# Performance work log

Hardware: AMD Instinct MI355X
Metric: run time of the kernel (lower is better)

Reference implementation:

```python
import jax, jax.numpy as jnp
import numpy as np

K, B, D, H, C, T = 3, 512, 1024, 512, 48, 25  # num_TAB, batch, linear_dim, hidden, n_classes, max_len

def setup_inputs() -> dict:
    key = jax.random.key(0)
    ks = jax.random.split(key, 18)
    rn = lambda k, s, sc=0.02: (jax.random.normal(k, s, jnp.float32) * sc)
    return {
        'S_ppps': jax.random.normal(ks[0], (K, B, D), jnp.float32),
        'R_ppps': jax.random.normal(ks[1], (K, B, D), jnp.float32),
        'cls_W': rn(ks[2], (K, 2 * D, C)), 'cls_b': jnp.zeros((K, C), jnp.float32),
        'dur_W': rn(ks[3], (K * D, 1)), 'dur_b': jnp.zeros((1,), jnp.float32),
        'lin_W': rn(ks[4], (2 * K * D + K * C, D + 1)), 'lin_b': jnp.zeros((D + 1,), jnp.float32),
        'W_ih': rn(ks[5], (4 * H, D + 1)), 'W_hh': rn(ks[6], (4 * H, H)),
        'b_ih': jnp.zeros((4 * H,), jnp.float32), 'b_hh': jnp.zeros((4 * H,), jnp.float32),
        'Wp': rn(ks[7], (H, C)), 'bp': jnp.zeros((C,), jnp.float32),
        'Wdur': rn(ks[8], (D + H, 1)), 'bdur': jnp.zeros((1,), jnp.float32),
        'embed': rn(ks[9], (C, D), 1.0),
        'Wattn': rn(ks[10], (H, D)),
    }

def reference(S_ppps, R_ppps, cls_W, cls_b, dur_W, dur_b, lin_W, lin_b,
              W_ih, W_hh, b_ih, b_hh, Wp, bp, Wdur, bdur, embed, Wattn):
    S_stack = jnp.transpose(S_ppps, (1, 0, 2))            # [B,K,D] (torch.stack(S_ppps,1))
    # per-TAB classifiers: Y[i] = softmax(Linear(cat(S_i,R_i)))
    SR = jnp.concatenate([S_ppps, R_ppps], axis=-1)       # [K,B,2D]
    Y = jax.nn.softmax(jnp.einsum('kbd,kdc->kbc', SR, cls_W) + cls_b[:, None, :], axis=-1)  # [K,B,C]
    Yf = jnp.transpose(Y, (1, 0, 2)).reshape(B, K * C)    # cat(Y0..Yk) feature-wise
    Sf = jnp.transpose(S_ppps, (1, 0, 2)).reshape(B, K * D)
    Rf = jnp.transpose(R_ppps, (1, 0, 2)).reshape(B, K * D)
    feat = jnp.concatenate([Yf, Sf, Rf], axis=1)          # [B, K*C + 2*K*D]
    x0 = feat @ lin_W + lin_b                             # [B, D+1]
    curr_dur = Rf @ dur_W + dur_b                         # [B,1]
    inv_sqrt_d = 1.0 / np.sqrt(D).astype(np.float32)

    def step(carry, _):
        x, h, c, prev_h = carry
        gates = x @ W_ih.T + b_ih + h @ W_hh.T + b_hh     # [B,4H], torch gate order i,f,g,o
        i_g, f_g, g_g, o_g = jnp.split(gates, 4, axis=1)
        c = jax.nn.sigmoid(f_g) * c + jax.nn.sigmoid(i_g) * jnp.tanh(g_g)
        h = jax.nn.sigmoid(o_g) * jnp.tanh(c)
        logits = h @ Wp + bp                              # [B,C]
        q = (h @ Wattn) * inv_sqrt_d                      # [B,D]
        aw = jax.nn.softmax(jnp.einsum('bd,bkd->bk', q, S_stack), axis=-1)
        att = jnp.einsum('bk,bkd->bd', aw, S_stack)       # [B,D]
        dur = jnp.concatenate([att, prev_h], axis=1) @ Wdur + bdur  # [B,1]
        labels = jnp.argmax(logits, axis=1)
        probs = jax.nn.softmax(logits, axis=1)
        nx = jnp.concatenate([embed[labels], dur], axis=1)  # [B,D+1]
        return (nx, h, c, h), (labels, probs, dur[:, 0], att)

    z = jnp.zeros((B, H), x0.dtype)
    _, (labels_t, probs_t, dur_t, att_t) = jax.lax.scan(step, (x0, z, z, z), None, length=T)
    curr_action = jnp.sum(Y, axis=0)                      # [B,C]
    pred_class_probs = jnp.transpose(probs_t, (1, 0, 2))  # [B,T,C]
    pred_action_durations = jnp.concatenate([curr_dur, dur_t.T], axis=1)  # [B,T+1]
    return (labels_t, pred_class_probs, curr_action, pred_action_durations, att_t)
```

## Files before the change

kernel.cpp:

```cpp
#include <hip/hip_runtime.h>
#include <math.h>

#define B 512
#define D 1024
#define H 512
#define C 48
#define K 3
#define T 25
#define DP1 1025
#define G4H 2048
#define NC 2112
#define NCV 2096
#define KP 1056
#define FK 6304

typedef _Float16 f16;
typedef _Float16 half8 __attribute__((ext_vector_type(8)));
typedef float floatx4 __attribute__((ext_vector_type(4)));

__device__ __forceinline__ float sigf(float x){ return 1.0f/(1.0f+expf(-x)); }


template<int MODE>
__device__ __forceinline__ void mf_load(
    const f16* __restrict__ Ahi, const f16* __restrict__ Alo,
    const f16* __restrict__ Bhi, const f16* __restrict__ Blo,
    int M, int lda, int ldb, int m0, int n0, int kbase, int k0, int t,
    const f16* __restrict__ Yh, const f16* __restrict__ Yl,
    const float* __restrict__ Sf, const float* __restrict__ Rf,
    half8& rah, half8& ral, half8& rbh, half8& rbl)
{
    int r = t>>2, seg = t&3;
    int kk = k0 + seg*8;
    {
        size_t off = (size_t)(n0+r)*ldb + kbase + kk;
        rbh = *(const half8*)(Bhi + off);
        rbl = *(const half8*)(Blo + off);
    }
    int m = m0 + r;
    if (MODE==0){
        if (m < M){
            size_t off = (size_t)m*lda + kbase + kk;
            rah = *(const half8*)(Ahi + off);
            ral = *(const half8*)(Alo + off);
        } else {
            #pragma unroll
            for (int i=0;i<8;i++){ rah[i]=(f16)0; ral[i]=(f16)0; }
        }
    } else {
        int kabs = kbase + kk;
        if (kabs < 144){
            rah = *(const half8*)(Yh + (size_t)m*144 + kabs);
            ral = *(const half8*)(Yl + (size_t)m*144 + kabs);
        } else if (kabs < 6288){
            int kp = kabs - 144;
            const float* src = (kp < 3*D)
                ? (Sf + (size_t)(kp>>10)*(B*D) + (size_t)m*D + (kp&(D-1)))
                : (Rf + (size_t)((kp-3*D)>>10)*(B*D) + (size_t)m*D + ((kp-3*D)&(D-1)));
            float4 f0 = *(const float4*)src;
            float4 f1 = *(const float4*)(src+4);
            float fv[8]={f0.x,f0.y,f0.z,f0.w,f1.x,f1.y,f1.z,f1.w};
            #pragma unroll
            for (int i=0;i<8;i++){
                f16 h=(f16)fv[i];
                rah[i]=h; ral[i]=(f16)(fv[i]-(float)h);
            }
        } else {
            #pragma unroll
            for (int i=0;i<8;i++){ rah[i]=(f16)0; ral[i]=(f16)0; }
        }
    }
}

template<int MODE>
__global__ __launch_bounds__(256)
void k_mfma(const f16* __restrict__ Ahi, const f16* __restrict__ Alo,
            const f16* __restrict__ Bhi, const f16* __restrict__ Blo,
            float* __restrict__ Cc, const float* __restrict__ bias,
            int M, int Nvalid, int Ktot, int lda, int ldb, int ldc,
            int ksl, size_t cstride, int MB, int Z, int zmaj,
            const f16* __restrict__ Yh, const f16* __restrict__ Yl,
            const float* __restrict__ Sf, const float* __restrict__ Rf)
{
    __shared__ __align__(16) f16 Ash[2][64][40];
    __shared__ __align__(16) f16 Asl[2][64][40];
    __shared__ __align__(16) f16 Bsh[2][64][40];
    __shared__ __align__(16) f16 Bsl[2][64][40];
    int t = threadIdx.x;
    int mblk, nblk, z;
    if (zmaj){
        z = blockIdx.x % Z;
        int rest = blockIdx.x / Z;
        mblk = rest % MB; nblk = rest / MB;
    } else {
        int chunk = gridDim.x >> 3;
        int g = (blockIdx.x & 7)*chunk + (blockIdx.x >> 3);
        int mz = g % (MB*Z);
        nblk = g / (MB*Z);
        mblk = mz / Z;
        z    = mz % Z;
    }
    int m0 = mblk*64, n0 = nblk*64;
    int kbase = z*ksl;
    int kcnt = (z==Z-1)? (Ktot-kbase) : ksl;
    int nIter = kcnt >> 5;
    int r = t>>2, seg = t&3;
    half8 rah, ral, rbh, rbl;
    mf_load<MODE>(Ahi,Alo,Bhi,Blo,M,lda,ldb,m0,n0,kbase,0,t,Yh,Yl,Sf,Rf,rah,ral,rbh,rbl);
    int lane = t&63, wv = t>>6;
    int lrow = lane&15, quad = lane>>4;
    floatx4 acc[4] = {};
    int cur = 0;
    for (int it=0; it<nIter; ++it){
        *(half8*)&Ash[cur][r][seg*8] = rah;
        *(half8*)&Asl[cur][r][seg*8] = ral;
        *(half8*)&Bsh[cur][r][seg*8] = rbh;
        *(half8*)&Bsl[cur][r][seg*8] = rbl;
        if (it+1 < nIter)
            mf_load<MODE>(Ahi,Alo,Bhi,Blo,M,lda,ldb,m0,n0,kbase,(it+1)<<5,t,Yh,Yl,Sf,Rf,rah,ral,rbh,rbl);
        __syncthreads();
        half8 ah = *(const half8*)&Ash[cur][wv*16+lrow][quad*8];
        half8 al = *(const half8*)&Asl[cur][wv*16+lrow][quad*8];
        #pragma unroll
        for (int j=0;j<4;j++){
            half8 bh = *(const half8*)&Bsh[cur][j*16+lrow][quad*8];
            half8 bl = *(const half8*)&Bsl[cur][j*16+lrow][quad*8];
            acc[j] = __builtin_amdgcn_mfma_f32_16x16x32_f16(ah, bh, acc[j], 0,0,0);
            acc[j] = __builtin_amdgcn_mfma_f32_16x16x32_f16(al, bh, acc[j], 0,0,0);
            acc[j] = __builtin_amdgcn_mfma_f32_16x16x32_f16(ah, bl, acc[j], 0,0,0);
        }
        cur ^= 1;
    }
    float* Cz = Cc + (size_t)z*cstride;
    #pragma unroll
    for (int j=0;j<4;j++){
        int col = n0 + j*16 + lrow;
        if (col >= Nvalid) continue;
        float bv = bias ? bias[col] : 0.f;
        #pragma unroll
        for (int i=0;i<4;i++){
            int row = m0 + wv*16 + quad*4 + i;
            if (row < M) Cz[(size_t)row*ldc + col] = acc[j][i] + bv;
        }
    }
}


__global__ void k_bt_build(const float* __restrict__ src, f16* __restrict__ hi, f16* __restrict__ lo,
                           int Ksrc, int Nsrc, int ld_src, int NB, int KB, float scale){
    __shared__ float tile[32][33];
    int k0 = blockIdx.x*32, n0 = blockIdx.y*32;
    int lx = threadIdx.x & 31, ly = threadIdx.x >> 5;
    for (int rr=0; rr<32; rr+=8){
        int k2 = k0+ly+rr, n = n0+lx;
        tile[ly+rr][lx] = (k2<Ksrc && n<Nsrc)? src[(size_t)k2*ld_src+n]*scale : 0.f;
    }
    __syncthreads();
    for (int rr=0; rr<32; rr+=8){
        int n = n0+ly+rr, k2 = k0+lx;
        if (n<NB && k2<KB){
            float v = tile[lx][ly+rr];
            f16 h=(f16)v;
            hi[(size_t)n*KB+k2]=h;
            lo[(size_t)n*KB+k2]=(f16)(v-(float)h);
        }
    }
}

__global__ void k_permrows(const float* __restrict__ src, f16* __restrict__ hi, f16* __restrict__ lo,
                           int src_ld, int dst_ld, int kvalid){
    int idx = blockIdx.x*256+threadIdx.x;
    if (idx >= G4H*dst_ld) return;
    int p = idx/dst_ld, k2 = idx%dst_ld;
    int j = p>>2, g = p&3, gi = (g<<9)|j;
    float v = (k2<kvalid)? src[(size_t)gi*src_ld + k2] : 0.f;
    f16 h=(f16)v;
    hi[idx]=h; lo[idx]=(f16)(v-(float)h);
}

__global__ void k_cvt(const float* __restrict__ src, f16* __restrict__ hi, f16* __restrict__ lo,
                      int M, int ld_src, int nvalid, int ld_dst, float scale){
    int idx = blockIdx.x*256+threadIdx.x;
    if (idx >= M*ld_dst) return;
    int m = idx/ld_dst, n = idx%ld_dst;
    float v = (n<nvalid)? src[(size_t)m*ld_src+n]*scale : 0.f;
    f16 h=(f16)v; hi[idx]=h; lo[idx]=(f16)(v-(float)h);
}

__global__ void k_cvtY(const float* __restrict__ Y, f16* __restrict__ hi, f16* __restrict__ lo){
    int idx = blockIdx.x*256+threadIdx.x;
    if (idx >= B*144) return;
    int b = idx/144, k2 = idx%144;
    float v = Y[((size_t)(k2/C)*B + b)*C + (k2%C)];
    f16 h=(f16)v; hi[idx]=h; lo[idx]=(f16)(v-(float)h);
}

__global__ void k_zeroh(f16* a, f16* b2, int n){
    int i = blockIdx.x*256+threadIdx.x; if (i<n){ a[i]=(f16)0; b2[i]=(f16)0; }
}

__global__ void k_prep(const float* __restrict__ bih, const float* __restrict__ bhh,
                       const float* __restrict__ bp, const float* __restrict__ Wih,
                       float* __restrict__ bias2p, float* __restrict__ biascat,
                       float* __restrict__ wl){
    int i = blockIdx.x*256 + threadIdx.x;
    if (i < G4H){
        int g=i&3, j=i>>2; int gi=(g<<9)|j;
        bias2p[i]=bih[gi]+bhh[gi];
        wl[i]=Wih[(size_t)gi*DP1 + 1024];
    }
    if (i < C) biascat[i]=bp[i];
}

__global__ void k_cls(const float* __restrict__ S, const float* __restrict__ R,
                      const float* __restrict__ clsW, const float* __restrict__ clsb,
                      float* __restrict__ Y){
    int kb = blockIdx.x; int k = kb / B; int b = kb % B;
    int t = threadIdx.x;
    __shared__ float sr[64];
    __shared__ float lg[C];
    __shared__ float mred[2];
    float acc = (t<C) ? clsb[k*C+t] : 0.f;
    const float* W = clsW + (size_t)k*2*D*C;
    for (int i0=0; i0<2*D; i0+=64){
        int i = i0 + t;
        sr[t] = (i < D) ? S[((size_t)k*B+b)*D + i] : R[((size_t)k*B+b)*D + (i-D)];
        __syncthreads();
        if (t < C){ for (int ii=0; ii<64; ++ii) acc += sr[ii]*W[(size_t)(i0+ii)*C + t]; }
        __syncthreads();
    }
    if (t<C) lg[t]=acc;
    __syncthreads();
    if (t==0){
        float m=lg[0]; for(int c2=1;c2<C;c2++) m=fmaxf(m,lg[c2]);
        float s=0.f; for(int c2=0;c2<C;c2++) s+=expf(lg[c2]-m);
        mred[0]=m; mred[1]=s;
    }
    __syncthreads();
    if (t<C) Y[((size_t)k*B+b)*C + t] = expf(lg[t]-mred[0])/mred[1];
}

__global__ void k_curr_action(const float* __restrict__ Y, float* __restrict__ outca){
    int i = blockIdx.x*256+threadIdx.x; if (i>=B*C) return;
    int b=i/C, c2=i%C;
    outca[i] = Y[((size_t)0*B+b)*C+c2] + Y[((size_t)1*B+b)*C+c2] + Y[((size_t)2*B+b)*C+c2];
}

__global__ void k_dur0(const float* __restrict__ R, const float* __restrict__ durW,
                       const float* __restrict__ durb, float* __restrict__ outpad){
    int b = blockIdx.x; int t = threadIdx.x;
    __shared__ float red[256];
    float p=0.f;
    for (int i=t; i<K*D; i+=256){ int k=i>>10, d=i&1023; p += R[((size_t)k*B+b)*D+d]*durW[i]; }
    red[t]=p; __syncthreads();
    for (int s=128;s>0;s>>=1){ if(t<s) red[t]+=red[t+s]; __syncthreads(); }
    if (t==0) outpad[(size_t)b*(T+1)] = red[0] + durb[0];
}

__global__ void k_red(float* __restrict__ dst, const float* __restrict__ src, int parts, size_t pstride,
                      int M, int Nld, int Nvalid, const float* __restrict__ bias){
    int idx = blockIdx.x*256+threadIdx.x;
    if (idx >= M*Nld) return;
    int n = idx % Nld;
    float v = 0.f;
    if (n < Nvalid){
        for (int p=0;p<parts;p++) v += src[(size_t)p*pstride + idx];
        if (bias) v += bias[n];
    }
    dst[idx]=v;
}

__global__ void k_redcvt(const float* __restrict__ src, int parts, size_t pstride,
                         const float* __restrict__ bias, f16* __restrict__ hi, f16* __restrict__ lo){
    int idx = blockIdx.x*256+threadIdx.x;
    if (idx >= 512*KP) return;
    int m = idx/KP, n = idx%KP;
    float v = 0.f;
    if (n < DP1){
        for (int p=0;p<parts;p++) v += src[(size_t)p*pstride + (size_t)m*1028 + n];
        v += bias[n];
    }
    f16 h=(f16)v; hi[idx]=h; lo[idx]=(f16)(v-(float)h);
}


__global__ void k_lstm0(const float* __restrict__ gxp, int parts, size_t pstride,
                        const float* __restrict__ bias2p,
                        float* __restrict__ c, f16* __restrict__ hhi, f16* __restrict__ hlo){
    int idx = blockIdx.x*256+threadIdx.x; if (idx>=B*H) return;
    int r=idx>>9, j=idx&511;
    float4 g = *(const float4*)&gxp[(size_t)r*G4H + (j<<2)];
    if (parts==2){
        float4 g2 = *(const float4*)&gxp[pstride + (size_t)r*G4H + (j<<2)];
        g.x+=g2.x; g.y+=g2.y; g.z+=g2.z; g.w+=g2.w;
    }
    float4 bb = *(const float4*)&bias2p[j<<2];
    g.x+=bb.x; g.y+=bb.y; g.z+=bb.z; g.w+=bb.w;
    float cn = sigf(g.x)*tanhf(g.z);
    c[idx]=cn;
    float hv = sigf(g.w)*tanhf(cn);
    f16 h=(f16)hv; hhi[idx]=h; hlo[idx]=(f16)(hv-(float)h);
}

template<int PARTS>
__global__ void k_postapply(const float* __restrict__ rawg, size_t pstride,
                       const float* __restrict__ S, const float* __restrict__ V,
                       const f16* __restrict__ hchi, const f16* __restrict__ hclo,
                       const f16* __restrict__ holdhi, const f16* __restrict__ holdlo,
                       const float* __restrict__ E, const float* __restrict__ wl,
                       const float* __restrict__ biascat,
                       const float* __restrict__ Wdur, const float* __restrict__ bdur,
                       float* __restrict__ outlab, float* __restrict__ outprobs,
                       float* __restrict__ outatt, float* __restrict__ outpad,
                       float* __restrict__ c, f16* __restrict__ hNhi, f16* __restrict__ hNlo,
                       int tstep, int doLstm)
{
    int b=blockIdx.x, t=threadIdx.x;
    int lane=t&63, wv=t>>6;
    __shared__ float aw[3];
    __shared__ float redw[4][8];
    __shared__ int sbest;
    __shared__ float sdv;
    const float* z0 = rawg + (size_t)b*NC;
    if (t<64){
        float lgv = -3.0e38f;
        if (t<C){
            float v = 0.f;
            #pragma unroll
            for (int p=0;p<PARTS;p++) v += z0[(size_t)p*pstride + G4H + t];
            lgv = v + biascat[t];
        }
        float m = lgv; int bi = t;
        #pragma unroll
        for (int s2=32;s2>0;s2>>=1){
            float om=__shfl_xor(m,s2); int ob=__shfl_xor(bi,s2);
            if (om>m || (om==m && ob<bi)){ m=om; bi=ob; }
        }
        float e=(t<C)? expf(lgv-m):0.f;
        float ss=e;
        #pragma unroll
        for (int s2=32;s2>0;s2>>=1) ss+=__shfl_xor(ss,s2);
        if (t<C) outprobs[(size_t)b*(T*C)+tstep*C+t]=e/ss;
        if (t==0){
            sbest=bi;
            outlab[(size_t)tstep*B+b]=(float)bi;
        }
    }
    float hv_t = (float)hchi[(size_t)b*H + t] + (float)hclo[(size_t)b*H + t];
    float p0 = hv_t * V[((size_t)(0*B+b))*H + t];
    float p1 = hv_t * V[((size_t)(1*B+b))*H + t];
    float p2 = hv_t * V[((size_t)(2*B+b))*H + t];
    #pragma unroll
    for (int s2=32;s2>0;s2>>=1){
        p0 += __shfl_xor(p0,s2); p1 += __shfl_xor(p1,s2); p2 += __shfl_xor(p2,s2);
    }
    if (lane==0){ redw[0][wv]=p0; redw[1][wv]=p1; redw[2][wv]=p2; }
    __syncthreads();
    if (t==0){
        float a0=0.f,a1=0.f,a2=0.f;
        #pragma unroll
        for (int w=0;w<8;w++){ a0+=redw[0][w]; a1+=redw[1][w]; a2+=redw[2][w]; }
        float m=fmaxf(a0,fmaxf(a1,a2));
        float e0=expf(a0-m), e1=expf(a1-m), e2=expf(a2-m);
        float si=1.f/(e0+e1+e2);
        aw[0]=e0*si; aw[1]=e1*si; aw[2]=e2*si;
    }
    __syncthreads();
    float a0=aw[0],a1=aw[1],a2=aw[2];
    const float* S0  = S + (size_t)b*D;
    const float* S1  = S0 + (size_t)B*D;
    const float* S2p = S1 + (size_t)B*D;
    float dp = 0.f;
    float* attp = outatt + (size_t)tstep*B*D + (size_t)b*D;
    {
        int d = t<<1;
        float2 s0 = *(const float2*)(S0+d);
        float2 s1 = *(const float2*)(S1+d);
        float2 s2 = *(const float2*)(S2p+d);
        float2 w2 = *(const float2*)(Wdur+d);
        float2 av;
        av.x = a0*s0.x+a1*s1.x+a2*s2.x;
        av.y = a0*s0.y+a1*s1.y+a2*s2.y;
        *(float2*)(attp+d) = av;
        dp += av.x*w2.x+av.y*w2.y;
    }
    if (holdhi){
        float hvo = (float)holdhi[(size_t)b*H+t] + (float)holdlo[(size_t)b*H+t];
        dp += hvo * Wdur[D+t];
    }
    #pragma unroll
    for (int s2=32;s2>0;s2>>=1) dp += __shfl_xor(dp,s2);
    if (lane==0) redw[3][wv]=dp;
    __syncthreads();
    if (t==0){
        float dv=0.f;
        #pragma unroll
        for (int w=0;w<8;w++) dv+=redw[3][w];
        dv += bdur[0];
        outpad[(size_t)b*(T+1)+tstep+1]=dv; sdv=dv;
    }
    __syncthreads();
    if (doLstm){
        int lb=sbest; float dv=sdv;
        int j=t;
        float4 g4 = *(const float4*)&z0[4*j];
        #pragma unroll
        for (int p=1;p<PARTS;p++){
            float4 h4 = *(const float4*)&z0[(size_t)p*pstride + 4*j];
            g4.x+=h4.x; g4.y+=h4.y; g4.z+=h4.z; g4.w+=h4.w;
        }
        float4 e4 = *(const float4*)&E[(size_t)lb*G4H+4*j];
        float4 w4 = *(const float4*)&wl[4*j];
        float gi = g4.x+e4.x+dv*w4.x;
        float gf = g4.y+e4.y+dv*w4.y;
        float gg = g4.z+e4.z+dv*w4.z;
        float go = g4.w+e4.w+dv*w4.w;
        size_t ci=(size_t)b*H+j;
        float cn = sigf(gf)*c[ci] + sigf(gi)*tanhf(gg);
        c[ci]=cn;
        float hv = sigf(go)*tanhf(cn);
        f16 hh=(f16)hv;
        hNhi[ci]=hh; hNlo[ci]=(f16)(hv-(float)hh);
    }
}


extern "C" void kernel_launch(void* const* d_in, const int* in_sizes, int n_in,
                              void* d_out, int out_size, void* d_ws, size_t ws_size,
                              hipStream_t stream) {
    const float* S    = (const float*)d_in[0];
    const float* R    = (const float*)d_in[1];
    const float* clsW = (const float*)d_in[2];
    const float* clsb = (const float*)d_in[3];
    const float* durW = (const float*)d_in[4];
    const float* durb = (const float*)d_in[5];
    const float* linW = (const float*)d_in[6];
    const float* linb = (const float*)d_in[7];
    const float* Wih  = (const float*)d_in[8];
    const float* Whh  = (const float*)d_in[9];
    const float* bih  = (const float*)d_in[10];
    const float* bhh  = (const float*)d_in[11];
    const float* Wp   = (const float*)d_in[12];
    const float* bp   = (const float*)d_in[13];
    const float* Wdur = (const float*)d_in[14];
    const float* bdur = (const float*)d_in[15];
    const float* embed= (const float*)d_in[16];
    const float* Wattn= (const float*)d_in[17];

    float* out = (float*)d_out;
    float* outlab   = out;
    float* outprobs = out + 12800;
    float* outca    = out + 627200;
    float* outpad   = out + 651776;
    float* outatt   = out + 665088;

    float* ws = (float*)d_ws;
    float* E       = ws + 0;
    float* wl      = ws + 98304;
    float* bias2p  = ws + 100352;
    float* biascat = ws + 102400;
    float* c       = ws + 102464;
    f16*   hAhi    = (f16*)(ws + 364608);
    f16*   hAlo    = (f16*)(ws + 495680);
    f16*   hBhi    = (f16*)(ws + 626752);
    f16*   hBlo    = (f16*)(ws + 757824);
    f16*   Yhi     = (f16*)(ws + 889920);
    f16*   Ylo     = (f16*)(ws + 926784);
    float* Y       = ws + 963648;
    f16*   watthi  = (f16*)(ws + 1037376);
    f16*   wattlo  = (f16*)(ws + 1299520);
    f16*   x0hi    = (f16*)(ws + 1563712);
    f16*   x0lo    = (f16*)(ws + 1834048);
    f16*   embhi   = (f16*)(ws + 2104384);
    f16*   emblo   = (f16*)(ws + 2129728);
    const size_t SB = 2155072;
    f16*   lwthi   = (f16*)(ws + SB);
    f16*   lwtlo   = (f16*)(ws + SB + 3429376);
    float* x0part  = ws + SB + 6858752;
    f16*   Wcthi   = (f16*)(ws + SB);
    f16*   Wctlo   = (f16*)(ws + SB + 540672);
    f16*   Shi     = (f16*)(ws + SB + 1081344);
    f16*   Slo     = (f16*)(ws + SB + 1867776);
    float* Vbuf    = ws + SB + 2654208;
    f16*   Wihphi  = (f16*)(ws + SB + 3440640);
    f16*   Wihplo  = (f16*)(ws + SB + 4521984);
    float* rawg    = ws + SB + 3440640;
    float* gpart   = ws + SB + 5603328;

    int ZX0, ksl_x0;
    if      (ws_size >= (size_t)52898048){ ZX0=8; ksl_x0=800;  }
    else if (ws_size >= (size_t)44476672){ ZX0=4; ksl_x0=1600; }
    else                                 { ZX0=2; ksl_x0=3168; }
    const int ZGX = 2, ksl_gx = 544;
    const int ZE  = 4, ksl_e  = 256;
    const int ZSC = 4, ksl_sc = 128;

    k_prep<<<8,256,0,stream>>>(bih,bhh,bp,Wih,bias2p,biascat,wl);
    k_cls<<<K*B,64,0,stream>>>(S,R,clsW,clsb,Y);
    k_curr_action<<<(B*C+255)/256,256,0,stream>>>(Y,outca);
    k_cvtY<<<(B*144+255)/256,256,0,stream>>>(Y,Yhi,Ylo);
    k_dur0<<<B,256,0,stream>>>(R,durW,durb,outpad);
    k_bt_build<<<dim3((FK+31)/32,(1088+31)/32),256,0,stream>>>(linW,lwthi,lwtlo,6288,1025,1025,1088,FK,1.f);
    k_mfma<1><<<8*17*ZX0,256,0,stream>>>(nullptr,nullptr,lwthi,lwtlo,x0part,nullptr,
                                         512,1028,FK,0,FK,1028,ksl_x0,(size_t)512*1028,8,ZX0,1,
                                         Yhi,Ylo,S,R);
    k_redcvt<<<(512*KP+255)/256,256,0,stream>>>(x0part,ZX0,(size_t)512*1028,linb,x0hi,x0lo);
    k_permrows<<<(G4H*KP+255)/256,256,0,stream>>>(Wih,Wihphi,Wihplo,DP1,KP,DP1);
    k_mfma<0><<<8*32*ZGX,256,0,stream>>>(x0hi,x0lo,Wihphi,Wihplo,gpart,nullptr,
                                         512,G4H,KP,KP,KP,G4H,ksl_gx,(size_t)512*G4H,8,ZGX,0,
                                         nullptr,nullptr,nullptr,nullptr);
    k_lstm0<<<(B*H+255)/256,256,0,stream>>>(gpart,ZGX,(size_t)512*G4H,bias2p,c,hAhi,hAlo);
    k_cvt<<<(48*KP+255)/256,256,0,stream>>>(embed,embhi,emblo,48,1024,1024,KP,1.f);
    k_mfma<0><<<1*32*ZE,256,0,stream>>>(embhi,emblo,Wihphi,Wihplo,gpart,nullptr,
                                        48,G4H,KP,KP,KP,G4H,ksl_e,(size_t)48*G4H,1,ZE,0,
                                        nullptr,nullptr,nullptr,nullptr);
    k_red<<<(48*G4H+255)/256,256,0,stream>>>(E,gpart,ZE,(size_t)48*G4H,48,G4H,G4H,bias2p);
    k_cvt<<<(1536*1024+255)/256,256,0,stream>>>(S,Shi,Slo,1536,1024,1024,1024,1.f);
    k_cvt<<<(512*1024+255)/256,256,0,stream>>>(Wattn,watthi,wattlo,512,1024,1024,1024,0.03125f);
    k_mfma<0><<<24*8,256,0,stream>>>(Shi,Slo,watthi,wattlo,Vbuf,nullptr,
                                     1536,512,1024,1024,1024,512,1024,0,24,1,0,
                                     nullptr,nullptr,nullptr,nullptr);
    k_permrows<<<(G4H*512+255)/256,256,0,stream>>>(Whh,Wcthi,Wctlo,H,H,H);
    k_bt_build<<<dim3(16,2),256,0,stream>>>(Wp,Wcthi+(size_t)2048*512,Wctlo+(size_t)2048*512,
                                            512,48,48,48,512,1.f);
    k_zeroh<<<32,256,0,stream>>>(Wcthi+(size_t)2096*512,Wctlo+(size_t)2096*512,16*512);

    size_t pstr = (size_t)512*NC;
    f16 *hCurHi=hAhi, *hCurLo=hAlo, *hPrvHi=hBhi, *hPrvLo=hBlo;
    for (int t=0;t<T;t++){
        k_mfma<0><<<8*33*ZSC,256,0,stream>>>(hCurHi,hCurLo,Wcthi,Wctlo,rawg,nullptr,
                                             512,NCV,H,H,H,NC,ksl_sc,pstr,8,ZSC,0,
                                             nullptr,nullptr,nullptr,nullptr);
        k_postapply<4><<<B,512,0,stream>>>(rawg,pstr,S,Vbuf,hCurHi,hCurLo,
                                        (t==0)?nullptr:hPrvHi,(t==0)?nullptr:hPrvLo,
                                        E,wl,biascat,Wdur,bdur,
                                        outlab,outprobs,outatt,outpad,
                                        c,hPrvHi,hPrvLo,t,(t<T-1)?1:0);
        f16* th=hPrvHi; hPrvHi=hCurHi; hCurHi=th;
        f16* tl=hPrvLo; hPrvLo=hCurLo; hCurLo=tl;
    }
}
```

Measured before the change: 975.0 us.

## Templatize GEMM tile width, drop split-K in LSTM step, fast transcendentals

Makes the MFMA GEMM's N tile width a template parameter and uses narrower 32-wide tiles with more blocks for the x0 projection and the per-step recurrent GEMM. The per-step GEMM drops its 4-way split-K, so postapply reads a single partial instead of summing four. MODE 1 now issues the float loads before the MFMA work and does the fp16 hi/lo conversion after it, to hide global-load latency. Also swaps expf/tanhf for __expf-based fast versions and replaces __syncthreads with an explicit lgkmcnt wait plus s_barrier, which may cost some accuracy.

```diff
diff --git a/kernel.cpp b/kernel.cpp
--- a/kernel.cpp
+++ b/kernel.cpp
@@ -18,63 +18,16 @@
 typedef _Float16 half8 __attribute__((ext_vector_type(8)));
 typedef float floatx4 __attribute__((ext_vector_type(4)));
 
-__device__ __forceinline__ float sigf(float x){ return 1.0f/(1.0f+expf(-x)); }
-
-
-template<int MODE>
-__device__ __forceinline__ void mf_load(
-    const f16* __restrict__ Ahi, const f16* __restrict__ Alo,
-    const f16* __restrict__ Bhi, const f16* __restrict__ Blo,
-    int M, int lda, int ldb, int m0, int n0, int kbase, int k0, int t,
-    const f16* __restrict__ Yh, const f16* __restrict__ Yl,
-    const float* __restrict__ Sf, const float* __restrict__ Rf,
-    half8& rah, half8& ral, half8& rbh, half8& rbl)
-{
-    int r = t>>2, seg = t&3;
-    int kk = k0 + seg*8;
-    {
-        size_t off = (size_t)(n0+r)*ldb + kbase + kk;
-        rbh = *(const half8*)(Bhi + off);
-        rbl = *(const half8*)(Blo + off);
-    }
-    int m = m0 + r;
-    if (MODE==0){
-        if (m < M){
-            size_t off = (size_t)m*lda + kbase + kk;
-            rah = *(const half8*)(Ahi + off);
-            ral = *(const half8*)(Alo + off);
-        } else {
-            #pragma unroll
-            for (int i=0;i<8;i++){ rah[i]=(f16)0; ral[i]=(f16)0; }
-        }
-    } else {
-        int kabs = kbase + kk;
-        if (kabs < 144){
-            rah = *(const half8*)(Yh + (size_t)m*144 + kabs);
-            ral = *(const half8*)(Yl + (size_t)m*144 + kabs);
-        } else if (kabs < 6288){
-            int kp = kabs - 144;
-            const float* src = (kp < 3*D)
-                ? (Sf + (size_t)(kp>>10)*(B*D) + (size_t)m*D + (kp&(D-1)))
-                : (Rf + (size_t)((kp-3*D)>>10)*(B*D) + (size_t)m*D + ((kp-3*D)&(D-1)));
-            float4 f0 = *(const float4*)src;
-            float4 f1 = *(const float4*)(src+4);
-            float fv[8]={f0.x,f0.y,f0.z,f0.w,f1.x,f1.y,f1.z,f1.w};
-            #pragma unroll
-            for (int i=0;i<8;i++){
-                f16 h=(f16)fv[i];
-                rah[i]=h; ral[i]=(f16)(fv[i]-(float)h);
-            }
-        } else {
-            #pragma unroll
-            for (int i=0;i<8;i++){ rah[i]=(f16)0; ral[i]=(f16)0; }
-        }
-    }
-}
-
-template<int MODE>
+__device__ __forceinline__ float sigf(float x){ return 1.0f/(1.0f+__expf(-x)); }
+__device__ __forceinline__ float tanhf_fast(float x){
+    float t = __expf(-2.0f*fabsf(x));
+    float r = (1.0f-t)/(1.0f+t);
+    return x<0.f ? -r : r;
+}
+
+template<int NT, int MODE>
 __global__ __launch_bounds__(256)
-void k_mfma(const f16* __restrict__ Ahi, const f16* __restrict__ Alo,
+void k_gemm(const f16* __restrict__ Ahi, const f16* __restrict__ Alo,
             const f16* __restrict__ Bhi, const f16* __restrict__ Blo,
             float* __restrict__ Cc, const float* __restrict__ bias,
             int M, int Nvalid, int Ktot, int lda, int ldb, int ldc,
@@ -84,8 +37,8 @@
 {
     __shared__ __align__(16) f16 Ash[2][64][40];
     __shared__ __align__(16) f16 Asl[2][64][40];
-    __shared__ __align__(16) f16 Bsh[2][64][40];
-    __shared__ __align__(16) f16 Bsl[2][64][40];
+    __shared__ __align__(16) f16 Bsh[2][NT][40];
+    __shared__ __align__(16) f16 Bsl[2][NT][40];
     int t = threadIdx.x;
     int mblk, nblk, z;
     if (zmaj){
@@ -100,40 +53,95 @@
         mblk = mz / Z;
         z    = mz % Z;
     }
-    int m0 = mblk*64, n0 = nblk*64;
+    int m0 = mblk*64, n0 = nblk*NT;
     int kbase = z*ksl;
     int kcnt = (z==Z-1)? (Ktot-kbase) : ksl;
     int nIter = kcnt >> 5;
     int r = t>>2, seg = t&3;
+    const bool ldB = (r < NT);
     half8 rah, ral, rbh, rbl;
-    mf_load<MODE>(Ahi,Alo,Bhi,Blo,M,lda,ldb,m0,n0,kbase,0,t,Yh,Yl,Sf,Rf,rah,ral,rbh,rbl);
+    float4 fA0, fA1;
+
+    auto LOAD = [&](int k0){
+        int kk = k0 + seg*8;
+        if (ldB){
+            size_t off = (size_t)(n0+r)*ldb + kbase + kk;
+            rbh = *(const half8*)(Bhi + off);
+            rbl = *(const half8*)(Blo + off);
+        }
+        int m = m0 + r;
+        if (MODE==0){
+            if (m < M){
+                size_t off = (size_t)m*lda + kbase + kk;
+                rah = *(const half8*)(Ahi + off);
+                ral = *(const half8*)(Alo + off);
+            } else {
+                #pragma unroll
+                for (int i=0;i<8;i++){ rah[i]=(f16)0; ral[i]=(f16)0; }
+            }
+        } else {
+            int kabs = kbase + kk;
+            if (kabs < 144){
+                rah = *(const half8*)(Yh + (size_t)m*144 + kabs);
+                ral = *(const half8*)(Yl + (size_t)m*144 + kabs);
+            } else if (kabs < 6288){
+                int kp = kabs - 144;
+                const float* src = (kp < 3*D)
+                    ? (Sf + (size_t)(kp>>10)*(B*D) + (size_t)m*D + (kp&(D-1)))
+                    : (Rf + (size_t)((kp-3*D)>>10)*(B*D) + (size_t)m*D + ((kp-3*D)&(D-1)));
+                fA0 = *(const float4*)src;
+                fA1 = *(const float4*)(src+4);
+            } else {
+                #pragma unroll
+                for (int i=0;i<8;i++){ rah[i]=(f16)0; ral[i]=(f16)0; }
+            }
+        }
+    };
+    auto CONV = [&](int k0){
+        int kk = k0 + seg*8;
+        int kabs = kbase + kk;
+        if (kabs >= 144 && kabs < 6288){
+            float fv[8]={fA0.x,fA0.y,fA0.z,fA0.w,fA1.x,fA1.y,fA1.z,fA1.w};
+            #pragma unroll
+            for (int i=0;i<8;i++){
+                f16 h=(f16)fv[i];
+                rah[i]=h; ral[i]=(f16)(fv[i]-(float)h);
+            }
+        }
+    };
+
+    LOAD(0);
+    if (MODE==1) CONV(0);
     int lane = t&63, wv = t>>6;
     int lrow = lane&15, quad = lane>>4;
-    floatx4 acc[4] = {};
+    floatx4 acc[NT/16] = {};
     int cur = 0;
     for (int it=0; it<nIter; ++it){
         *(half8*)&Ash[cur][r][seg*8] = rah;
         *(half8*)&Asl[cur][r][seg*8] = ral;
-        *(half8*)&Bsh[cur][r][seg*8] = rbh;
-        *(half8*)&Bsl[cur][r][seg*8] = rbl;
-        if (it+1 < nIter)
-            mf_load<MODE>(Ahi,Alo,Bhi,Blo,M,lda,ldb,m0,n0,kbase,(it+1)<<5,t,Yh,Yl,Sf,Rf,rah,ral,rbh,rbl);
-        __syncthreads();
+        if (ldB){
+            *(half8*)&Bsh[cur][r][seg*8] = rbh;
+            *(half8*)&Bsl[cur][r][seg*8] = rbl;
+        }
+        if (it+1 < nIter) LOAD((it+1)<<5);
+        asm volatile("s_waitcnt lgkmcnt(0)" ::: "memory");
+        __builtin_amdgcn_s_barrier();
         half8 ah = *(const half8*)&Ash[cur][wv*16+lrow][quad*8];
         half8 al = *(const half8*)&Asl[cur][wv*16+lrow][quad*8];
         #pragma unroll
-        for (int j=0;j<4;j++){
+        for (int j=0;j<NT/16;j++){
             half8 bh = *(const half8*)&Bsh[cur][j*16+lrow][quad*8];
             half8 bl = *(const half8*)&Bsl[cur][j*16+lrow][quad*8];
             acc[j] = __builtin_amdgcn_mfma_f32_16x16x32_f16(ah, bh, acc[j], 0,0,0);
             acc[j] = __builtin_amdgcn_mfma_f32_16x16x32_f16(al, bh, acc[j], 0,0,0);
             acc[j] = __builtin_amdgcn_mfma_f32_16x16x32_f16(ah, bl, acc[j], 0,0,0);
         }
+        if (MODE==1 && it+1 < nIter) CONV((it+1)<<5);
         cur ^= 1;
     }
     float* Cz = Cc + (size_t)z*cstride;
     #pragma unroll
-    for (int j=0;j<4;j++){
+    for (int j=0;j<NT/16;j++){
         int col = n0 + j*16 + lrow;
         if (col >= Nvalid) continue;
         float bv = bias ? bias[col] : 0.f;
@@ -296,9 +304,9 @@
     }
     float4 bb = *(const float4*)&bias2p[j<<2];
     g.x+=bb.x; g.y+=bb.y; g.z+=bb.z; g.w+=bb.w;
-    float cn = sigf(g.x)*tanhf(g.z);
+    float cn = sigf(g.x)*tanhf_fast(g.z);
     c[idx]=cn;
-    float hv = sigf(g.w)*tanhf(cn);
+    float hv = sigf(g.w)*tanhf_fast(cn);
     f16 h=(f16)hv; hhi[idx]=h; hlo[idx]=(f16)(hv-(float)h);
 }
 
@@ -336,7 +344,7 @@
             float om=__shfl_xor(m,s2); int ob=__shfl_xor(bi,s2);
             if (om>m || (om==m && ob<bi)){ m=om; bi=ob; }
         }
-        float e=(t<C)? expf(lgv-m):0.f;
+        float e=(t<C)? __expf(lgv-m):0.f;
         float ss=e;
         #pragma unroll
         for (int s2=32;s2>0;s2>>=1) ss+=__shfl_xor(ss,s2);
@@ -361,7 +369,7 @@
         #pragma unroll
         for (int w=0;w<8;w++){ a0+=redw[0][w]; a1+=redw[1][w]; a2+=redw[2][w]; }
         float m=fmaxf(a0,fmaxf(a1,a2));
-        float e0=expf(a0-m), e1=expf(a1-m), e2=expf(a2-m);
+        float e0=__expf(a0-m), e1=__expf(a1-m), e2=__expf(a2-m);
         float si=1.f/(e0+e1+e2);
         aw[0]=e0*si; aw[1]=e1*si; aw[2]=e2*si;
     }
@@ -416,9 +424,9 @@
         float gg = g4.z+e4.z+dv*w4.z;
         float go = g4.w+e4.w+dv*w4.w;
         size_t ci=(size_t)b*H+j;
-        float cn = sigf(gf)*c[ci] + sigf(gi)*tanhf(gg);
+        float cn = sigf(gf)*c[ci] + sigf(gi)*tanhf_fast(gg);
         c[ci]=cn;
-        float hv = sigf(go)*tanhf(cn);
+        float hv = sigf(go)*tanhf_fast(cn);
         f16 hh=(f16)hv;
         hNhi[ci]=hh; hNlo[ci]=(f16)(hv-(float)hh);
     }
@@ -493,7 +501,6 @@
     else                                 { ZX0=2; ksl_x0=3168; }
     const int ZGX = 2, ksl_gx = 544;
     const int ZE  = 4, ksl_e  = 256;
-    const int ZSC = 4, ksl_sc = 128;
 
     k_prep<<<8,256,0,stream>>>(bih,bhh,bp,Wih,bias2p,biascat,wl);
     k_cls<<<K*B,64,0,stream>>>(S,R,clsW,clsb,Y);
@@ -501,25 +508,25 @@
     k_cvtY<<<(B*144+255)/256,256,0,stream>>>(Y,Yhi,Ylo);
     k_dur0<<<B,256,0,stream>>>(R,durW,durb,outpad);
     k_bt_build<<<dim3((FK+31)/32,(1088+31)/32),256,0,stream>>>(linW,lwthi,lwtlo,6288,1025,1025,1088,FK,1.f);
-    k_mfma<1><<<8*17*ZX0,256,0,stream>>>(nullptr,nullptr,lwthi,lwtlo,x0part,nullptr,
-                                         512,1028,FK,0,FK,1028,ksl_x0,(size_t)512*1028,8,ZX0,1,
-                                         Yhi,Ylo,S,R);
+    k_gemm<32,1><<<8*33*ZX0,256,0,stream>>>(nullptr,nullptr,lwthi,lwtlo,x0part,nullptr,
+                                            512,1028,FK,0,FK,1028,ksl_x0,(size_t)512*1028,8,ZX0,1,
+                                            Yhi,Ylo,S,R);
     k_redcvt<<<(512*KP+255)/256,256,0,stream>>>(x0part,ZX0,(size_t)512*1028,linb,x0hi,x0lo);
     k_permrows<<<(G4H*KP+255)/256,256,0,stream>>>(Wih,Wihphi,Wihplo,DP1,KP,DP1);
-    k_mfma<0><<<8*32*ZGX,256,0,stream>>>(x0hi,x0lo,Wihphi,Wihplo,gpart,nullptr,
-                                         512,G4H,KP,KP,KP,G4H,ksl_gx,(size_t)512*G4H,8,ZGX,0,
-                                         nullptr,nullptr,nullptr,nullptr);
+    k_gemm<64,0><<<8*32*ZGX,256,0,stream>>>(x0hi,x0lo,Wihphi,Wihplo,gpart,nullptr,
+                                            512,G4H,KP,KP,KP,G4H,ksl_gx,(size_t)512*G4H,8,ZGX,0,
+                                            nullptr,nullptr,nullptr,nullptr);
     k_lstm0<<<(B*H+255)/256,256,0,stream>>>(gpart,ZGX,(size_t)512*G4H,bias2p,c,hAhi,hAlo);
     k_cvt<<<(48*KP+255)/256,256,0,stream>>>(embed,embhi,emblo,48,1024,1024,KP,1.f);
-    k_mfma<0><<<1*32*ZE,256,0,stream>>>(embhi,emblo,Wihphi,Wihplo,gpart,nullptr,
-                                        48,G4H,KP,KP,KP,G4H,ksl_e,(size_t)48*G4H,1,ZE,0,
-                                        nullptr,nullptr,nullptr,nullptr);
+    k_gemm<64,0><<<1*32*ZE,256,0,stream>>>(embhi,emblo,Wihphi,Wihplo,gpart,nullptr,
+                                           48,G4H,KP,KP,KP,G4H,ksl_e,(size_t)48*G4H,1,ZE,0,
+                                           nullptr,nullptr,nullptr,nullptr);
     k_red<<<(48*G4H+255)/256,256,0,stream>>>(E,gpart,ZE,(size_t)48*G4H,48,G4H,G4H,bias2p);
     k_cvt<<<(1536*1024+255)/256,256,0,stream>>>(S,Shi,Slo,1536,1024,1024,1024,1.f);
     k_cvt<<<(512*1024+255)/256,256,0,stream>>>(Wattn,watthi,wattlo,512,1024,1024,1024,0.03125f);
-    k_mfma<0><<<24*8,256,0,stream>>>(Shi,Slo,watthi,wattlo,Vbuf,nullptr,
-                                     1536,512,1024,1024,1024,512,1024,0,24,1,0,
-                                     nullptr,nullptr,nullptr,nullptr);
+    k_gemm<64,0><<<24*8,256,0,stream>>>(Shi,Slo,watthi,wattlo,Vbuf,nullptr,
+                                        1536,512,1024,1024,1024,512,1024,0,24,1,0,
+                                        nullptr,nullptr,nullptr,nullptr);
     k_permrows<<<(G4H*512+255)/256,256,0,stream>>>(Whh,Wcthi,Wctlo,H,H,H);
     k_bt_build<<<dim3(16,2),256,0,stream>>>(Wp,Wcthi+(size_t)2048*512,Wctlo+(size_t)2048*512,
                                             512,48,48,48,512,1.f);
@@ -528,10 +535,10 @@
     size_t pstr = (size_t)512*NC;
     f16 *hCurHi=hAhi, *hCurLo=hAlo, *hPrvHi=hBhi, *hPrvLo=hBlo;
     for (int t=0;t<T;t++){
-        k_mfma<0><<<8*33*ZSC,256,0,stream>>>(hCurHi,hCurLo,Wcthi,Wctlo,rawg,nullptr,
-                                             512,NCV,H,H,H,NC,ksl_sc,pstr,8,ZSC,0,
-                                             nullptr,nullptr,nullptr,nullptr);
-        k_postapply<4><<<B,512,0,stream>>>(rawg,pstr,S,Vbuf,hCurHi,hCurLo,
+        k_gemm<32,0><<<8*66,256,0,stream>>>(hCurHi,hCurLo,Wcthi,Wctlo,rawg,nullptr,
+                                            512,NCV,H,H,H,NC,512,pstr,8,1,0,
+                                            nullptr,nullptr,nullptr,nullptr);
+        k_postapply<1><<<B,512,0,stream>>>(rawg,pstr,S,Vbuf,hCurHi,hCurLo,
                                         (t==0)?nullptr:hPrvHi,(t==0)?nullptr:hPrvLo,
                                         E,wl,biascat,Wdur,bdur,
                                         outlab,outprobs,outatt,outpad,
```

Result: faster. 859.3 us (-11.9%).
